# Optimization experiments

Measured on AMD Instinct MI355X. Metric: run time of the kernel, lower is better.

The kernel has to match this reference:

```python
import jax, jax.numpy as jnp
import numpy as np

B, L, C, R = 4, 2048, 64, 8
A_SCALE = 0.1  # keeps spectral radius of per-step A < 1 so 2048-step products stay stable


def setup_inputs() -> dict:
    key = jax.random.key(0)
    k1, k2, k3, k4 = jax.random.split(key, 4)
    A_re = jax.random.normal(k1, (B, L, C, R, R), jnp.float32) * A_SCALE
    A_im = jax.random.normal(k2, (B, L, C, R, R), jnp.float32) * A_SCALE
    X_re = jax.random.normal(k3, (B, L, C, R), jnp.float32)
    X_im = jax.random.normal(k4, (B, L, C, R), jnp.float32)
    return {"A_re": A_re, "A_im": A_im, "X_re": X_re, "X_im": X_im}


def reference(A_re, A_im, X_re, X_im):
    # Complex linear recurrence: Y_t = A_t @ Y_{t-1} + X_t (Y_0 = X_0),
    # computed as a parallel associative scan over the L axis, matching
    # the Triton combine_fn: (a1,x1) o (a2,x2) = (a2@a1, a2@x1 + x2).
    A = jax.lax.complex(A_re, A_im)  # [B,L,C,R,R] complex64
    X = jax.lax.complex(X_re, X_im)  # [B,L,C,R]   complex64

    def combine(left, right):
        a1, x1 = left
        a2, x2 = right
        new_a = jnp.matmul(a2, a1)                          # [.,R,R]@[.,R,R]
        new_x = jnp.einsum('...ij,...j->...i', a2, x1) + x2  # [.,R,R]@[.,R]
        return (new_a, new_x)

    _, Y = jax.lax.associative_scan(combine, (A, X), axis=1)
    # Return real/imag stacked so the output dtype is float32: [B,L,C,R,2]
    return jnp.stack((jnp.real(Y), jnp.imag(Y)), axis=-1)
```

## Files before the change

kernel.cpp:

```cpp
#include <hip/hip_runtime.h>

#define B 4
#define L 2048
#define C 64
#define R 8
#define NCH (B * C)
#define TQ 16
#define S (L / TQ)
#define GRP (NCH / 8)


__global__ __launch_bounds__(256) void k_summary(
    const float* __restrict__ Are, const float* __restrict__ Aim,
    const float* __restrict__ Xre, const float* __restrict__ Xim,
    float2* __restrict__ sumP, float2* __restrict__ sumQ)
{
    __shared__ __align__(16) float sm[4 * 2 * 1248];
    const int lane = threadIdx.x & 63;
    const int w = __builtin_amdgcn_readfirstlane((int)(threadIdx.x >> 6));
    const int c = lane >> 3, r = lane & 7;
    const int s = blockIdx.x >> 3;
    const int g = (blockIdx.x & 7) * 4 + w;
    const int n0 = g * 8;
    const int b = n0 >> 6;
    const int cc0 = n0 & (C - 1);
    const int n = n0 + c;
    const int tbase = s * TQ;

    char* const smw = ((char*)sm) + w * 9984;
    char* const wrA = smw + 272 * c + 32 * r;
    char* const wrX = smw + 4352 + 80 * c + 4 * r;
    const char* const rdA = smw + 272 * c;
    const char* const rdX = smw + 4352 + 80 * c;

    const int fb0 = (b * L + (tbase + TQ - 1)) * C + cc0;
    const float* pA  = Are + (long)fb0 * 64 + lane * 8;
    const float* pI  = Aim + (long)fb0 * 64 + lane * 8;
    const float* pXr = Xre + (long)fb0 * 8 + lane;
    const float* pXi = Xim + (long)fb0 * 8 + lane;

    float Pre[8], Pim[8], Nre[8], Nim[8];
#pragma unroll
    for (int k = 0; k < 8; ++k) { Pre[k] = (k == r) ? 1.f : 0.f; Pim[k] = 0.f; }
    float qre = 0.f, qim = 0.f;

    float4 sa0, sa1, si0, si1; float sxr, sxi;
    float4 ta0, ta1, ti0, ti1; float txr, txi;

#define SLOAD(A0, A1, I0, I1, XR, XI)                                          \
    {                                                                          \
        A0 = *(const float4*)pA; A1 = *(const float4*)(pA + 4);                \
        I0 = *(const float4*)pI; I1 = *(const float4*)(pI + 4);                \
        XR = *pXr; XI = *pXi;                                                  \
        pA -= 4096; pI -= 4096; pXr -= 512; pXi -= 512;                        \
    }

#define SSTAGE(BUF, A0, A1, I0, I1, XR, XI)                                    \
    {                                                                          \
        *(float4*)(wrA + (BUF)) = A0;                                          \
        *(float4*)(wrA + (BUF) + 16) = A1;                                     \
        *(float4*)(wrA + (BUF) + 2176) = I0;                                   \
        *(float4*)(wrA + (BUF) + 2176 + 16) = I1;                              \
        *(float*)(wrX + (BUF)) = XR;                                           \
        *(float*)(wrX + (BUF) + 32) = XI;                                      \
    }

#define SCOMP(BUF, SRe, SIm, DRe, DIm)                                         \
    {                                                                          \
        float xr[8], xi[8];                                                    \
        *(float4*)&xr[0] = *(const float4*)(rdX + (BUF));                      \
        *(float4*)&xr[4] = *(const float4*)(rdX + (BUF) + 16);                 \
        *(float4*)&xi[0] = *(const float4*)(rdX + (BUF) + 32);                 \
        *(float4*)&xi[4] = *(const float4*)(rdX + (BUF) + 48);                 \
        _Pragma("unroll")                                                      \
        for (int k = 0; k < 8; ++k) {                                          \
            qre += SRe[k] * xr[k] - SIm[k] * xi[k];                            \
            qim += SRe[k] * xi[k] + SIm[k] * xr[k];                            \
        }                                                                      \
        _Pragma("unroll")                                                      \
        for (int j = 0; j < 8; ++j) { DRe[j] = 0.f; DIm[j] = 0.f; }            \
        _Pragma("unroll")                                                      \
        for (int k = 0; k < 8; ++k) {                                          \
            float er[8], ei[8];                                                \
            *(float4*)&er[0] = *(const float4*)(rdA + (BUF) + 32 * k);         \
            *(float4*)&er[4] = *(const float4*)(rdA + (BUF) + 32 * k + 16);    \
            *(float4*)&ei[0] = *(const float4*)(rdA + (BUF) + 2176 + 32 * k);  \
            *(float4*)&ei[4] = *(const float4*)(rdA + (BUF) + 2192 + 32 * k);  \
            const float pr = SRe[k], pi = SIm[k];                              \
            _Pragma("unroll")                                                  \
            for (int j = 0; j < 8; ++j) {                                      \
                DRe[j] += pr * er[j] - pi * ei[j];                             \
                DIm[j] += pr * ei[j] + pi * er[j];                             \
            }                                                                  \
        }                                                                      \
    }

    SLOAD(sa0, sa1, si0, si1, sxr, sxi);
    SLOAD(ta0, ta1, ti0, ti1, txr, txi);

#pragma unroll 1
    for (int tt = TQ - 1; tt >= 1; tt -= 2) {
        SSTAGE(0, sa0, sa1, si0, si1, sxr, sxi);
        if (tt >= 3) SLOAD(sa0, sa1, si0, si1, sxr, sxi);
        SCOMP(0, Pre, Pim, Nre, Nim);
        SSTAGE(4992, ta0, ta1, ti0, ti1, txr, txi);
        if (tt >= 3) SLOAD(ta0, ta1, ti0, ti1, txr, txi);
        SCOMP(4992, Nre, Nim, Pre, Pim);
    }

    float4* gp = (float4*)(sumP + ((long)(s * 256 + n) * 8 + r) * 8);
    gp[0] = make_float4(Pre[0], Pim[0], Pre[1], Pim[1]);
    gp[1] = make_float4(Pre[2], Pim[2], Pre[3], Pim[3]);
    gp[2] = make_float4(Pre[4], Pim[4], Pre[5], Pim[5]);
    gp[3] = make_float4(Pre[6], Pim[6], Pre[7], Pim[7]);
    sumQ[(long)(s * 256 + n) * 8 + r] = make_float2(qre, qim);
}

__global__ __launch_bounds__(64) void k_carry(
    const float2* __restrict__ sumP, const float2* __restrict__ sumQ,
    float2* __restrict__ carry)
{
    const int lane = threadIdx.x;
    const int c = lane >> 3, r = lane & 7;
    const int n = blockIdx.x * 8 + c;
    const long base2 = (long)n * 8;

    float yr = 0.f, yi = 0.f;

    float4 A0,A1,A2,A3, B0,B1,B2,B3, C0,C1,C2,C3, D0,D1,D2,D3;
    float2 Aq, Bq, Cq, Dq;

#define CLOAD(P0,P1,P2,P3,QV,SS)                                               \
    {                                                                          \
        const float4* np = (const float4*)(sumP + (base2 + (long)(SS) * 2048 + r) * 8); \
        P0 = np[0]; P1 = np[1]; P2 = np[2]; P3 = np[3];                        \
        QV = sumQ[base2 + (long)(SS) * 2048 + r];                              \
    }

#define CSTEP(P0,P1,P2,P3,QV,SS)                                               \
    {                                                                          \
        carry[base2 + (long)(SS) * 2048 + r] = make_float2(yr, yi);            \
        float4 w0 = P0, w1 = P1, w2 = P2, w3 = P3;                             \
        float2 qs = QV;                                                        \
        if ((SS) + 4 < S) CLOAD(P0,P1,P2,P3,QV,(SS) + 4);                      \
        float yvr[8], yvi[8];                                                  \
        _Pragma("unroll")                                                      \
        for (int k = 0; k < 8; ++k) {                                          \
            yvr[k] = __shfl(yr, (c << 3) + k, 64);                             \
            yvi[k] = __shfl(yi, (c << 3) + k, 64);                             \
        }                                                                      \
        float prr[8], pri[8];                                                  \
        prr[0]=w0.x; pri[0]=w0.y; prr[1]=w0.z; pri[1]=w0.w;                    \
        prr[2]=w1.x; pri[2]=w1.y; prr[3]=w1.z; pri[3]=w1.w;                    \
        prr[4]=w2.x; pri[4]=w2.y; prr[5]=w2.z; pri[5]=w2.w;                    \
        prr[6]=w3.x; pri[6]=w3.y; prr[7]=w3.z; pri[7]=w3.w;                    \
        float nr0 = qs.x, ni0 = qs.y, nr1 = 0.f, ni1 = 0.f;                    \
        _Pragma("unroll")                                                      \
        for (int k = 0; k < 8; k += 2) {                                       \
            nr0 += prr[k] * yvr[k] - pri[k] * yvi[k];                          \
            ni0 += prr[k] * yvi[k] + pri[k] * yvr[k];                          \
            nr1 += prr[k+1] * yvr[k+1] - pri[k+1] * yvi[k+1];                  \
            ni1 += prr[k+1] * yvi[k+1] + pri[k+1] * yvr[k+1];                  \
        }                                                                      \
        yr = nr0 + nr1; yi = ni0 + ni1;                                        \
    }

    CLOAD(A0,A1,A2,A3,Aq, 0);
    CLOAD(B0,B1,B2,B3,Bq, 1);
    CLOAD(C0,C1,C2,C3,Cq, 2);
    CLOAD(D0,D1,D2,D3,Dq, 3);

#pragma unroll 1
    for (int ss = 0; ss < S; ss += 4) {
        CSTEP(A0,A1,A2,A3,Aq, ss);
        CSTEP(B0,B1,B2,B3,Bq, ss + 1);
        CSTEP(C0,C1,C2,C3,Cq, ss + 2);
        CSTEP(D0,D1,D2,D3,Dq, ss + 3);
    }
}

__global__ __launch_bounds__(256) void k_fixup(
    const float* __restrict__ Are, const float* __restrict__ Aim,
    const float* __restrict__ Xre, const float* __restrict__ Xim,
    const float2* __restrict__ carry, float2* __restrict__ out)
{
    const int lane = threadIdx.x & 63;
    const int w = threadIdx.x >> 6;
    const int c = lane >> 3, r = lane & 7;
    const int blk = (int)gridDim.x - 1 - (int)blockIdx.x;
    const int s = blk >> 3;
    const int g = (blk & 7) * 4 + w;
    const int n0 = g * 8;
    const int b = n0 >> 6;
    const int cc0 = n0 & (C - 1);
    const int n = n0 + c;
    const int tbase = s * TQ;

    float yvr[8], yvi[8];
    {
        const float4* cv = (const float4*)(carry + (long)(s * 256 + n) * 8);
        float4 w0 = cv[0], w1 = cv[1], w2 = cv[2], w3 = cv[3];
        yvr[0]=w0.x; yvi[0]=w0.y; yvr[1]=w0.z; yvi[1]=w0.w;
        yvr[2]=w1.x; yvi[2]=w1.y; yvr[3]=w1.z; yvi[3]=w1.w;
        yvr[4]=w2.x; yvi[4]=w2.y; yvr[5]=w2.z; yvi[5]=w2.w;
        yvr[6]=w3.x; yvi[6]=w3.y; yvr[7]=w3.z; yvi[7]=w3.w;
    }

    float4 sa0, sa1, si0, si1; float sxr, sxi;
    float4 ta0, ta1, ti0, ti1; float txr, txi;

#define LOADSET3(t, A0, A1, I0, I1, XR, XI)                                    \
    {                                                                          \
        const int fb = (b * L + (t)) * C + cc0;                                \
        const float4* pA = (const float4*)(Are + (long)fb * 64) + lane * 2;    \
        const float4* pI = (const float4*)(Aim + (long)fb * 64) + lane * 2;    \
        A0 = pA[0]; A1 = pA[1]; I0 = pI[0]; I1 = pI[1];                        \
        XR = Xre[(long)fb * 8 + lane]; XI = Xim[(long)fb * 8 + lane];          \
    }

#define FIX_STEP(A0, A1, I0, I1, XR_, XI_, t)                                  \
    {                                                                          \
        float nr0 = (XR_), ni0 = (XI_), nr1 = 0.f, ni1 = 0.f;                  \
        nr0 += A0.x * yvr[0] - I0.x * yvi[0];                                  \
        ni0 += A0.x * yvi[0] + I0.x * yvr[0];                                  \
        nr1 += A0.y * yvr[1] - I0.y * yvi[1];                                  \
        ni1 += A0.y * yvi[1] + I0.y * yvr[1];                                  \
        nr0 += A0.z * yvr[2] - I0.z * yvi[2];                                  \
        ni0 += A0.z * yvi[2] + I0.z * yvr[2];                                  \
        nr1 += A0.w * yvr[3] - I0.w * yvi[3];                                  \
        ni1 += A0.w * yvi[3] + I0.w * yvr[3];                                  \
        nr0 += A1.x * yvr[4] - I1.x * yvi[4];                                  \
        ni0 += A1.x * yvi[4] + I1.x * yvr[4];                                  \
        nr1 += A1.y * yvr[5] - I1.y * yvi[5];                                  \
        ni1 += A1.y * yvi[5] + I1.y * yvr[5];                                  \
        nr0 += A1.z * yvr[6] - I1.z * yvi[6];                                  \
        ni0 += A1.z * yvi[6] + I1.z * yvr[6];                                  \
        nr1 += A1.w * yvr[7] - I1.w * yvi[7];                                  \
        ni1 += A1.w * yvi[7] + I1.w * yvr[7];                                  \
        const float nr = nr0 + nr1, ni = ni0 + ni1;                            \
        const int fb = (b * L + (t)) * C + cc0;                                \
        out[(long)fb * 8 + lane] = make_float2(nr, ni);                        \
        _Pragma("unroll")                                                      \
        for (int k = 0; k < 8; ++k) {                                          \
            yvr[k] = __shfl(nr, (c << 3) + k, 64);                             \
            yvi[k] = __shfl(ni, (c << 3) + k, 64);                             \
        }                                                                      \
    }

    LOADSET3(tbase + 0, sa0, sa1, si0, si1, sxr, sxi);
    LOADSET3(tbase + 1, ta0, ta1, ti0, ti1, txr, txi);

#pragma unroll 1
    for (int tt = 0; tt < TQ; tt += 2) {
        float4 A0 = sa0, A1 = sa1, I0 = si0, I1 = si1;
        float XR = sxr, XI = sxi;
        if (tt + 2 < TQ) LOADSET3(tbase + tt + 2, sa0, sa1, si0, si1, sxr, sxi);
        FIX_STEP(A0, A1, I0, I1, XR, XI, tbase + tt);
        float4 B0 = ta0, B1 = ta1, J0 = ti0, J1 = ti1;
        float YR = txr, YI = txi;
        if (tt + 3 < TQ) LOADSET3(tbase + tt + 3, ta0, ta1, ti0, ti1, txr, txi);
        FIX_STEP(B0, B1, J0, J1, YR, YI, tbase + tt + 1);
    }
}

extern "C" void kernel_launch(void* const* d_in, const int* in_sizes, int n_in,
                              void* d_out, int out_size, void* d_ws, size_t ws_size,
                              hipStream_t stream)
{
    const float* Are = (const float*)d_in[0];
    const float* Aim = (const float*)d_in[1];
    const float* Xre = (const float*)d_in[2];
    const float* Xim = (const float*)d_in[3];
    float2* out = (float2*)d_out;

    float2* sumP  = (float2*)d_ws;
    float2* sumQ  = sumP + (long)S * NCH * 64;
    float2* carry = sumQ + (long)S * NCH * 8;

    k_summary<<<(S * GRP) / 4, 256, 0, stream>>>(Are, Aim, Xre, Xim, sumP, sumQ);
    k_carry<<<NCH / 8, 64, 0, stream>>>(sumP, sumQ, carry);
    k_fixup<<<(S * GRP) / 4, 256, 0, stream>>>(Are, Aim, Xre, Xim, carry, out);
}
```

Measured before the change: 409.9 us.

## Deepen software pipelining in summary and fixup kernels

The summary kernel now stages the first two steps into shared memory before the loop and puts the compute ahead of the next stage/load inside the loop, with a peeled epilogue, so loads for later steps run during the matrix products. The fixup kernel moves from a two-step to a four-step register prefetch ring, so global loads for step t+4 are in flight while step t is computed. The aim is to hide global memory latency in both latency-bound sequential loops. The cost is more registers in the fixup kernel, which may lower occupancy.

```diff
diff --git a/kernel.cpp b/kernel.cpp
--- a/kernel.cpp
+++ b/kernel.cpp
@@ -97,16 +97,26 @@
 
     SLOAD(sa0, sa1, si0, si1, sxr, sxi);
     SLOAD(ta0, ta1, ti0, ti1, txr, txi);
+    SSTAGE(0, sa0, sa1, si0, si1, sxr, sxi);
+    SLOAD(sa0, sa1, si0, si1, sxr, sxi);
+    SSTAGE(4992, ta0, ta1, ti0, ti1, txr, txi);
+    SLOAD(ta0, ta1, ti0, ti1, txr, txi);
 
 #pragma unroll 1
-    for (int tt = TQ - 1; tt >= 1; tt -= 2) {
+    for (int tt = TQ - 1; tt >= 5; tt -= 2) {
+        SCOMP(0, Pre, Pim, Nre, Nim);
         SSTAGE(0, sa0, sa1, si0, si1, sxr, sxi);
-        if (tt >= 3) SLOAD(sa0, sa1, si0, si1, sxr, sxi);
-        SCOMP(0, Pre, Pim, Nre, Nim);
+        SLOAD(sa0, sa1, si0, si1, sxr, sxi);
+        SCOMP(4992, Nre, Nim, Pre, Pim);
         SSTAGE(4992, ta0, ta1, ti0, ti1, txr, txi);
-        if (tt >= 3) SLOAD(ta0, ta1, ti0, ti1, txr, txi);
-        SCOMP(4992, Nre, Nim, Pre, Pim);
-    }
+        SLOAD(ta0, ta1, ti0, ti1, txr, txi);
+    }
+    SCOMP(0, Pre, Pim, Nre, Nim);
+    SSTAGE(0, sa0, sa1, si0, si1, sxr, sxi);
+    SCOMP(4992, Nre, Nim, Pre, Pim);
+    SSTAGE(4992, ta0, ta1, ti0, ti1, txr, txi);
+    SCOMP(0, Pre, Pim, Nre, Nim);
+    SCOMP(4992, Nre, Nim, Pre, Pim);
 
     float4* gp = (float4*)(sumP + ((long)(s * 256 + n) * 8 + r) * 8);
     gp[0] = make_float4(Pre[0], Pim[0], Pre[1], Pim[1]);
@@ -206,10 +216,12 @@
         yvr[6]=w3.x; yvi[6]=w3.y; yvr[7]=w3.z; yvi[7]=w3.w;
     }
 
-    float4 sa0, sa1, si0, si1; float sxr, sxi;
-    float4 ta0, ta1, ti0, ti1; float txr, txi;
-
-#define LOADSET3(t, A0, A1, I0, I1, XR, XI)                                    \
+    float4 Ua0,Ua1,Ui0,Ui1; float Uxr,Uxi;
+    float4 Va0,Va1,Vi0,Vi1; float Vxr,Vxi;
+    float4 Wa0,Wa1,Wi0,Wi1; float Wxr,Wxi;
+    float4 Za0,Za1,Zi0,Zi1; float Zxr,Zxi;
+
+#define FLOAD(t, A0, A1, I0, I1, XR, XI)                                       \
     {                                                                          \
         const int fb = (b * L + (t)) * C + cc0;                                \
         const float4* pA = (const float4*)(Are + (long)fb * 64) + lane * 2;    \
@@ -247,19 +259,21 @@
         }                                                                      \
     }
 
-    LOADSET3(tbase + 0, sa0, sa1, si0, si1, sxr, sxi);
-    LOADSET3(tbase + 1, ta0, ta1, ti0, ti1, txr, txi);
+    FLOAD(tbase + 0, Ua0,Ua1,Ui0,Ui1,Uxr,Uxi);
+    FLOAD(tbase + 1, Va0,Va1,Vi0,Vi1,Vxr,Vxi);
+    FLOAD(tbase + 2, Wa0,Wa1,Wi0,Wi1,Wxr,Wxi);
+    FLOAD(tbase + 3, Za0,Za1,Zi0,Zi1,Zxr,Zxi);
 
 #pragma unroll 1
-    for (int tt = 0; tt < TQ; tt += 2) {
-        float4 A0 = sa0, A1 = sa1, I0 = si0, I1 = si1;
-        float XR = sxr, XI = sxi;
-        if (tt + 2 < TQ) LOADSET3(tbase + tt + 2, sa0, sa1, si0, si1, sxr, sxi);
-        FIX_STEP(A0, A1, I0, I1, XR, XI, tbase + tt);
-        float4 B0 = ta0, B1 = ta1, J0 = ti0, J1 = ti1;
-        float YR = txr, YI = txi;
-        if (tt + 3 < TQ) LOADSET3(tbase + tt + 3, ta0, ta1, ti0, ti1, txr, txi);
-        FIX_STEP(B0, B1, J0, J1, YR, YI, tbase + tt + 1);
+    for (int tt = 0; tt < TQ; tt += 4) {
+        FIX_STEP(Ua0,Ua1,Ui0,Ui1,Uxr,Uxi, tbase + tt);
+        if (tt + 4 < TQ) FLOAD(tbase + tt + 4, Ua0,Ua1,Ui0,Ui1,Uxr,Uxi);
+        FIX_STEP(Va0,Va1,Vi0,Vi1,Vxr,Vxi, tbase + tt + 1);
+        if (tt + 5 < TQ) FLOAD(tbase + tt + 5, Va0,Va1,Vi0,Vi1,Vxr,Vxi);
+        FIX_STEP(Wa0,Wa1,Wi0,Wi1,Wxr,Wxi, tbase + tt + 2);
+        if (tt + 6 < TQ) FLOAD(tbase + tt + 6, Wa0,Wa1,Wi0,Wi1,Wxr,Wxi);
+        FIX_STEP(Za0,Za1,Zi0,Zi1,Zxr,Zxi, tbase + tt + 3);
+        if (tt + 7 < TQ) FLOAD(tbase + tt + 7, Za0,Za1,Zi0,Zi1,Zxr,Zxi);
     }
 }
 
```

Result: no change. 409.0 us (-0.2%).
